# Performance work log

Hardware: AMD Instinct MI355X
Metric: run time of the kernel (lower is better)

## Reference

```python
import jax, jax.numpy as jnp
import numpy as np

B, S, E, H = 1, 4096, 768, 12
D = E // H  # head_dim = 64


def setup_inputs() -> dict:
    key = jax.random.key(0)
    ks = jax.random.split(key, 9)
    s = 1.0 / np.sqrt(E)
    return {
        "x": jax.random.normal(ks[0], (B, S, E), dtype=jnp.float32),
        "Wq": jax.random.uniform(ks[1], (E, E), jnp.float32, -s, s),
        "bq": jax.random.uniform(ks[2], (E,), jnp.float32, -s, s),
        "Wk": jax.random.uniform(ks[3], (E, E), jnp.float32, -s, s),
        "bk": jax.random.uniform(ks[4], (E,), jnp.float32, -s, s),
        "Wv": jax.random.uniform(ks[5], (E, E), jnp.float32, -s, s),
        "bv": jax.random.uniform(ks[6], (E,), jnp.float32, -s, s),
        "Wo": jax.random.uniform(ks[7], (E, E), jnp.float32, -s, s),
        "bo": jax.random.uniform(ks[8], (E,), jnp.float32, -s, s),
    }


def reference(x, Wq, bq, Wk, bk, Wv, bv, Wo, bo):
    b, s, e = x.shape
    # QKV projections, split heads -> [b, h, s, d]
    def split(t):
        return t.reshape(b, s, H, D).transpose(0, 2, 1, 3)
    q = split(x @ Wq.T + bq)
    k = split(x @ Wk.T + bk)
    v = split(x @ Wv.T + bv)
    scores = jnp.einsum("bhqd,bhkd->bhqk", q, k) / jnp.sqrt(jnp.float32(D))
    attn = jax.nn.softmax(scores, axis=-1)  # dropout is identity in eval
    out = jnp.einsum("bhqk,bhkd->bhqd", attn, v)
    out = out.transpose(0, 2, 1, 3).reshape(b, s, e)
    return out @ Wo.T + bo
```

## Files before the change

### kernel.cpp

```cpp
#include <hip/hip_runtime.h>
#include <hip/hip_bf16.h>
#include <math.h>

#define SEQ 4096
#define EDIM 768
#define NHEAD 12
#define HDIM 64
#define SE (SEQ * EDIM)
#define WMAT (EDIM * EDIM)
#define QSCALE 0.180336880111f

typedef __attribute__((ext_vector_type(8))) __bf16 bf16x8;
typedef __attribute__((ext_vector_type(4))) float f32x4;
typedef __attribute__((ext_vector_type(8))) unsigned short u16x8;
typedef unsigned short ushort_t;
typedef unsigned int uint_t;

#define MFMA16(a, b, c) __builtin_amdgcn_mfma_f32_16x16x32_bf16(a, b, c, 0, 0, 0)
#define GLOAD_LDS16(g, l)                                          \
  __builtin_amdgcn_global_load_lds(                                \
      (const __attribute__((address_space(1))) void*)(g),          \
      (__attribute__((address_space(3))) void*)(l), 16, 0, 0)

__device__ __forceinline__ unsigned short bfbits(float x) {
  return __builtin_bit_cast(unsigned short, (__bf16)x);
}
__device__ __forceinline__ void split1(float x, unsigned short* h,
                                       unsigned short* l) {
  __bf16 hb = (__bf16)x;
  *h = __builtin_bit_cast(unsigned short, hb);
  *l = __builtin_bit_cast(unsigned short, (__bf16)(x - (float)hb));
}
__device__ __forceinline__ bf16x8 ones8() {
  u16x8 u;
#pragma unroll
  for (int e = 0; e < 8; ++e) u[e] = 0x3F80;
  return __builtin_bit_cast(bf16x8, u);
}

__global__ __launch_bounds__(256) void wprep_kernel(
    const float* __restrict__ W0, const float* __restrict__ W1,
    const float* __restrict__ W2, const float* __restrict__ W3,
    ushort_t* __restrict__ WB, ushort_t* __restrict__ WOH,
    ushort_t* __restrict__ WOL) {
  const int m = blockIdx.y;
  const float* src = (m == 0) ? W0 : (m == 1) ? W1 : (m == 2) ? W2 : W3;
  const size_t i = ((size_t)blockIdx.x * 256 + threadIdx.x) * 8;
  float4 a = *(const float4*)(src + i);
  float4 b = *(const float4*)(src + i + 4);
  float fv[8] = {a.x, a.y, a.z, a.w, b.x, b.y, b.z, b.w};
  if (m < 3) {
    u16x8 hh;
#pragma unroll
    for (int e = 0; e < 8; ++e) hh[e] = bfbits(fv[e]);
    *(u16x8*)(WB + (size_t)m * WMAT + i) = hh;
  } else {
    u16x8 hh, ll;
#pragma unroll
    for (int e = 0; e < 8; ++e) {
      unsigned short x, y;
      split1(fv[e], &x, &y);
      hh[e] = x;
      ll[e] = y;
    }
    *(u16x8*)(WOH + i) = hh;
    *(u16x8*)(WOL + i) = ll;
  }
}

__global__ __launch_bounds__(256) void xprep_kernel(
    const float* __restrict__ x, ushort_t* __restrict__ xb) {
  const size_t i = ((size_t)blockIdx.x * 256 + threadIdx.x) * 8;
  float4 a = *(const float4*)(x + i);
  float4 b = *(const float4*)(x + i + 4);
  float fv[8] = {a.x, a.y, a.z, a.w, b.x, b.y, b.z, b.w};
  u16x8 hh;
#pragma unroll
  for (int e = 0; e < 8; ++e) hh[e] = bfbits(fv[e]);
  *(u16x8*)(xb + i) = hh;
}

__global__ __launch_bounds__(256) void qkv_kernel(
    const ushort_t* __restrict__ XB, const ushort_t* __restrict__ WB,
    const float* __restrict__ bq, const float* __restrict__ bk,
    const float* __restrict__ bv, ushort_t* __restrict__ QB,
    ushort_t* __restrict__ KB, ushort_t* __restrict__ VB) {
  __shared__ __align__(16) ushort_t AS[128][32];
  __shared__ __align__(16) ushort_t BS[128][32];

  const int z = blockIdx.z;
  const ushort_t* Bmat = WB + (size_t)z * WMAT;
  const float* bias = (z == 0) ? bq : (z == 1) ? bk : bv;
  ushort_t* outp = (z == 0) ? QB : (z == 1) ? KB : VB;
  const float scale = (z == 0) ? QSCALE : 1.0f;

  const int t = threadIdx.x;
  const int lane = t & 63;
  const int w = t >> 6;
  const int tn = t & 15;
  const int g = (t >> 4) & 3;
  const int wr = w >> 1, wc = w & 1;
  const int m0 = blockIdx.x * 128;
  const int n0 = blockIdx.y * 128;

  f32x4 acc[4][4];
#pragma unroll
  for (int mi = 0; mi < 4; ++mi)
#pragma unroll
    for (int nj = 0; nj < 4; ++nj) acc[mi][nj] = (f32x4){0.f, 0.f, 0.f, 0.f};

  const int crow = lane >> 2;
  const int ccol = (lane & 3) * 8;

  for (int k0 = 0; k0 < EDIM; k0 += 32) {
    __syncthreads();
#pragma unroll
    for (int i = 0; i < 2; ++i) {
      const int ch = w + 4 * i;
      const int row = ch * 16 + crow;
      GLOAD_LDS16(XB + (size_t)(m0 + row) * EDIM + k0 + ccol, &AS[ch * 16][0]);
      GLOAD_LDS16(Bmat + (size_t)(n0 + row) * EDIM + k0 + ccol, &BS[ch * 16][0]);
    }
    __syncthreads();

    bf16x8 ah[4], bh[4];
#pragma unroll
    for (int mi = 0; mi < 4; ++mi)
      ah[mi] = __builtin_bit_cast(
          bf16x8, *(const u16x8*)&AS[wr * 64 + mi * 16 + tn][8 * g]);
#pragma unroll
    for (int nj = 0; nj < 4; ++nj)
      bh[nj] = __builtin_bit_cast(
          bf16x8, *(const u16x8*)&BS[wc * 64 + nj * 16 + tn][8 * g]);
#pragma unroll
    for (int mi = 0; mi < 4; ++mi)
#pragma unroll
      for (int nj = 0; nj < 4; ++nj)
        acc[mi][nj] = MFMA16(ah[mi], bh[nj], acc[mi][nj]);
  }

#pragma unroll
  for (int mi = 0; mi < 4; ++mi) {
    const int rb = m0 + wr * 64 + mi * 16 + 4 * g;
#pragma unroll
    for (int nj = 0; nj < 4; ++nj) {
      const int col = n0 + wc * 64 + nj * 16 + tn;
      const float bb = bias[col];
#pragma unroll
      for (int r = 0; r < 4; ++r)
        outp[(size_t)(rb + r) * EDIM + col] =
            bfbits((acc[mi][nj][r] + bb) * scale);
    }
  }
}

__global__ __launch_bounds__(256) void proj_kernel(
    const ushort_t* __restrict__ Ah, const ushort_t* __restrict__ Al,
    const ushort_t* __restrict__ Bh, const ushort_t* __restrict__ Bl,
    const float* __restrict__ bias, float* __restrict__ outf) {
  __shared__ __align__(16) ushort_t AhS[128][32];
  __shared__ __align__(16) ushort_t AlS[128][32];
  __shared__ __align__(16) ushort_t BhS[128][32];
  __shared__ __align__(16) ushort_t BlS[128][32];

  const int t = threadIdx.x;
  const int lane = t & 63;
  const int w = t >> 6;
  const int tn = t & 15;
  const int g = (t >> 4) & 3;
  const int wr = w >> 1, wc = w & 1;
  const int m0 = blockIdx.x * 128;
  const int n0 = blockIdx.y * 128;

  f32x4 acc[4][4];
#pragma unroll
  for (int mi = 0; mi < 4; ++mi)
#pragma unroll
    for (int nj = 0; nj < 4; ++nj) acc[mi][nj] = (f32x4){0.f, 0.f, 0.f, 0.f};

  const int crow = lane >> 2;
  const int ccol = (lane & 3) * 8;

  for (int k0 = 0; k0 < EDIM; k0 += 32) {
    __syncthreads();
#pragma unroll
    for (int i = 0; i < 2; ++i) {
      const int ch = w + 4 * i;
      const int row = ch * 16 + crow;
      const size_t ga = (size_t)(m0 + row) * EDIM + k0 + ccol;
      const size_t gb = (size_t)(n0 + row) * EDIM + k0 + ccol;
      GLOAD_LDS16(Ah + ga, &AhS[ch * 16][0]);
      GLOAD_LDS16(Al + ga, &AlS[ch * 16][0]);
      GLOAD_LDS16(Bh + gb, &BhS[ch * 16][0]);
      GLOAD_LDS16(Bl + gb, &BlS[ch * 16][0]);
    }
    __syncthreads();

    bf16x8 ah[4], al[4], bh[4], bl[4];
#pragma unroll
    for (int mi = 0; mi < 4; ++mi) {
      ah[mi] = __builtin_bit_cast(
          bf16x8, *(const u16x8*)&AhS[wr * 64 + mi * 16 + tn][8 * g]);
      al[mi] = __builtin_bit_cast(
          bf16x8, *(const u16x8*)&AlS[wr * 64 + mi * 16 + tn][8 * g]);
    }
#pragma unroll
    for (int nj = 0; nj < 4; ++nj) {
      bh[nj] = __builtin_bit_cast(
          bf16x8, *(const u16x8*)&BhS[wc * 64 + nj * 16 + tn][8 * g]);
      bl[nj] = __builtin_bit_cast(
          bf16x8, *(const u16x8*)&BlS[wc * 64 + nj * 16 + tn][8 * g]);
    }
#pragma unroll
    for (int mi = 0; mi < 4; ++mi)
#pragma unroll
      for (int nj = 0; nj < 4; ++nj)
        acc[mi][nj] = MFMA16(ah[mi], bh[nj], acc[mi][nj]);
#pragma unroll
    for (int mi = 0; mi < 4; ++mi)
#pragma unroll
      for (int nj = 0; nj < 4; ++nj)
        acc[mi][nj] = MFMA16(al[mi], bh[nj], acc[mi][nj]);
#pragma unroll
    for (int mi = 0; mi < 4; ++mi)
#pragma unroll
      for (int nj = 0; nj < 4; ++nj)
        acc[mi][nj] = MFMA16(ah[mi], bl[nj], acc[mi][nj]);
  }

#pragma unroll
  for (int mi = 0; mi < 4; ++mi) {
    const int rb = m0 + wr * 64 + mi * 16 + 4 * g;
#pragma unroll
    for (int nj = 0; nj < 4; ++nj) {
      const int col = n0 + wc * 64 + nj * 16 + tn;
      const float bb = bias[col];
#pragma unroll
      for (int r = 0; r < 4; ++r)
        outf[(size_t)(rb + r) * EDIM + col] = acc[mi][nj][r] + bb;
    }
  }
}

__global__ __launch_bounds__(256) void attn_kernel(
    const ushort_t* __restrict__ QB, const ushort_t* __restrict__ KBg,
    const ushort_t* __restrict__ Vg, ushort_t* __restrict__ Ch_g,
    ushort_t* __restrict__ Cl_g) {
  constexpr int DP = HDIM + 8;
  __shared__ __align__(16) ushort_t KS[64][DP];
  __shared__ __align__(16) ushort_t Vt[HDIM][DP];
  __shared__ __align__(16) ushort_t Ps[4][16][DP];

  const int t = threadIdx.x;
  const int tn = t & 15;
  const int g = (t >> 4) & 3;
  const int kg = g * 8;
  const int wid = t >> 6;
  const int h = blockIdx.y;
  const int q0 = blockIdx.x * 64;
  const int hoff = h * HDIM;

  bf16x8 qb[2];
  {
    const size_t qoff = (size_t)(q0 + 16 * wid + tn) * EDIM + hoff;
#pragma unroll
    for (int st = 0; st < 2; ++st)
      qb[st] = __builtin_bit_cast(bf16x8,
                                  *(const u16x8*)(QB + qoff + 32 * st + kg));
  }

  const int kr = t >> 2;
  const int kc = (t & 3) * 16;
  const int vkey = (t & 31) * 2;
  const int vd0 = (t >> 5) * 8;

  u16x8 kh0, kh1, vv0, vv1;
  {
    const size_t ko = (size_t)kr * EDIM + hoff + kc;
    kh0 = *(const u16x8*)(KBg + ko);
    kh1 = *(const u16x8*)(KBg + ko + 8);
    const size_t vo = (size_t)vkey * EDIM + hoff + vd0;
    vv0 = *(const u16x8*)(Vg + vo);
    vv1 = *(const u16x8*)(Vg + vo + EDIM);
  }

  const bf16x8 ones = ones8();
  f32x4 o[4], lsum;
#pragma unroll
  for (int j = 0; j < 4; ++j) o[j] = (f32x4){0.f, 0.f, 0.f, 0.f};
  lsum = (f32x4){0.f, 0.f, 0.f, 0.f};

  for (int k0 = 0; k0 < SEQ; k0 += 64) {
    __syncthreads();
    *(u16x8*)&KS[kr][kc] = kh0;
    *(u16x8*)&KS[kr][kc + 8] = kh1;
#pragma unroll
    for (int i = 0; i < 8; ++i) {
      const uint_t wv = (uint_t)vv0[i] | ((uint_t)vv1[i] << 16);
      *(uint_t*)&Vt[vd0 + i][vkey] = wv;
    }
    if (k0 + 64 < SEQ) {
      const size_t ko = (size_t)(k0 + 64 + kr) * EDIM + hoff + kc;
      kh0 = *(const u16x8*)(KBg + ko);
      kh1 = *(const u16x8*)(KBg + ko + 8);
      const size_t vo = (size_t)(k0 + 64 + vkey) * EDIM + hoff + vd0;
      vv0 = *(const u16x8*)(Vg + vo);
      vv1 = *(const u16x8*)(Vg + vo + EDIM);
    }
    __syncthreads();

    f32x4 s[4];
#pragma unroll
    for (int j = 0; j < 4; ++j) s[j] = (f32x4){0.f, 0.f, 0.f, 0.f};
#pragma unroll
    for (int j = 0; j < 4; ++j)
#pragma unroll
      for (int st = 0; st < 2; ++st) {
        const bf16x8 kb = __builtin_bit_cast(
            bf16x8, *(const u16x8*)&KS[j * 16 + tn][32 * st + kg]);
        s[j] = MFMA16(qb[st], kb, s[j]);
      }

#pragma unroll
    for (int r = 0; r < 4; ++r)
#pragma unroll
      for (int j = 0; j < 4; ++j)
        Ps[wid][4 * g + r][16 * j + tn] = bfbits(exp2f(s[j][r]));

    bf16x8 pa[2];
#pragma unroll
    for (int st = 0; st < 2; ++st)
      pa[st] = __builtin_bit_cast(
          bf16x8, *(const u16x8*)&Ps[wid][tn][32 * st + kg]);
#pragma unroll
    for (int j = 0; j < 4; ++j)
#pragma unroll
      for (int st = 0; st < 2; ++st) {
        const bf16x8 vb = __builtin_bit_cast(
            bf16x8, *(const u16x8*)&Vt[j * 16 + tn][32 * st + kg]);
        o[j] = MFMA16(pa[st], vb, o[j]);
      }
    lsum = MFMA16(pa[0], ones, lsum);
    lsum = MFMA16(pa[1], ones, lsum);
  }

#pragma unroll
  for (int r = 0; r < 4; ++r) {
    const float inv = 1.f / lsum[r];
#pragma unroll
    for (int j = 0; j < 4; ++j) {
      const float val = o[j][r] * inv;
      unsigned short hh, ll;
      split1(val, &hh, &ll);
      const size_t idx =
          (size_t)(q0 + 16 * wid + 4 * g + r) * EDIM + hoff + 16 * j + tn;
      Ch_g[idx] = hh;
      Cl_g[idx] = ll;
    }
  }
}

extern "C" void kernel_launch(void* const* d_in, const int* in_sizes, int n_in,
                              void* d_out, int out_size, void* d_ws,
                              size_t ws_size, hipStream_t stream) {
  const float* x  = (const float*)d_in[0];
  const float* Wq = (const float*)d_in[1];
  const float* bq = (const float*)d_in[2];
  const float* Wk = (const float*)d_in[3];
  const float* bk = (const float*)d_in[4];
  const float* Wv = (const float*)d_in[5];
  const float* bv = (const float*)d_in[6];
  const float* Wo = (const float*)d_in[7];
  const float* bo = (const float*)d_in[8];
  float* out = (float*)d_out;

  ushort_t* WB  = (ushort_t*)d_ws;
  ushort_t* WOH = WB + (size_t)3 * WMAT;
  ushort_t* WOL = WOH + (size_t)WMAT;
  ushort_t* XB  = WOL + (size_t)WMAT;
  ushort_t* QB  = XB + (size_t)SE;
  ushort_t* KB  = QB + (size_t)SE;
  ushort_t* VB  = KB + (size_t)SE;
  ushort_t* CH  = VB + (size_t)SE;
  ushort_t* CL  = CH + (size_t)SE;

  dim3 gw(WMAT / 2048, 4);
  wprep_kernel<<<gw, 256, 0, stream>>>(Wq, Wk, Wv, Wo, WB, WOH, WOL);
  xprep_kernel<<<SE / 2048, 256, 0, stream>>>(x, XB);

  dim3 gq(SEQ / 128, EDIM / 128, 3);
  qkv_kernel<<<gq, 256, 0, stream>>>(XB, WB, bq, bk, bv, QB, KB, VB);

  dim3 ga(SEQ / 64, NHEAD);
  attn_kernel<<<ga, 256, 0, stream>>>(QB, KB, VB, CH, CL);

  dim3 go(SEQ / 128, EDIM / 128);
  proj_kernel<<<go, 256, 0, stream>>>(CH, CL, WOH, WOL, bo, out);
}
```

Measured before the change: 177.5 us.

## Halve attention block to two waves with 32 query rows each and double-buffered K/V

```diff
diff --git a/kernel.cpp b/kernel.cpp
--- a/kernel.cpp
+++ b/kernel.cpp
@@ -242,14 +242,14 @@
   }
 }
 
-__global__ __launch_bounds__(256) void attn_kernel(
+__global__ __launch_bounds__(128) void attn_kernel(
     const ushort_t* __restrict__ QB, const ushort_t* __restrict__ KBg,
     const ushort_t* __restrict__ Vg, ushort_t* __restrict__ Ch_g,
     ushort_t* __restrict__ Cl_g) {
   constexpr int DP = HDIM + 8;
-  __shared__ __align__(16) ushort_t KS[64][DP];
-  __shared__ __align__(16) ushort_t Vt[HDIM][DP];
-  __shared__ __align__(16) ushort_t Ps[4][16][DP];
+  __shared__ __align__(16) ushort_t KS[2][64][DP];
+  __shared__ __align__(16) ushort_t Vt[2][HDIM][DP];
+  __shared__ __align__(16) ushort_t Ps[2][32][DP];
 
   const int t = threadIdx.x;
   const int tn = t & 15;
@@ -260,104 +260,138 @@
   const int q0 = blockIdx.x * 64;
   const int hoff = h * HDIM;
 
-  bf16x8 qb[2];
+  bf16x8 qb[2][2];
+#pragma unroll
+  for (int rb = 0; rb < 2; ++rb) {
+    const size_t qoff =
+        (size_t)(q0 + 32 * wid + 16 * rb + tn) * EDIM + hoff;
+#pragma unroll
+    for (int st = 0; st < 2; ++st)
+      qb[rb][st] = __builtin_bit_cast(
+          bf16x8, *(const u16x8*)(QB + qoff + 32 * st + kg));
+  }
+
+  const int kr = t >> 1;
+  const int kc = (t & 1) * 32;
+  const int vkey = (t & 31) * 2;
+  const int vd0 = ((t >> 5) & 3) * 16;
+
+  u16x8 kreg[4], vreg[4];
   {
-    const size_t qoff = (size_t)(q0 + 16 * wid + tn) * EDIM + hoff;
-#pragma unroll
-    for (int st = 0; st < 2; ++st)
-      qb[st] = __builtin_bit_cast(bf16x8,
-                                  *(const u16x8*)(QB + qoff + 32 * st + kg));
-  }
-
-  const int kr = t >> 2;
-  const int kc = (t & 3) * 16;
-  const int vkey = (t & 31) * 2;
-  const int vd0 = (t >> 5) * 8;
-
-  u16x8 kh0, kh1, vv0, vv1;
-  {
-    const size_t ko = (size_t)kr * EDIM + hoff + kc;
-    kh0 = *(const u16x8*)(KBg + ko);
-    kh1 = *(const u16x8*)(KBg + ko + 8);
-    const size_t vo = (size_t)vkey * EDIM + hoff + vd0;
-    vv0 = *(const u16x8*)(Vg + vo);
-    vv1 = *(const u16x8*)(Vg + vo + EDIM);
+    const ushort_t* kp = KBg + (size_t)kr * EDIM + hoff + kc;
+    kreg[0] = *(const u16x8*)kp;
+    kreg[1] = *(const u16x8*)(kp + 8);
+    kreg[2] = *(const u16x8*)(kp + 16);
+    kreg[3] = *(const u16x8*)(kp + 24);
+    const ushort_t* vp = Vg + (size_t)vkey * EDIM + hoff + vd0;
+    vreg[0] = *(const u16x8*)vp;
+    vreg[1] = *(const u16x8*)(vp + 8);
+    vreg[2] = *(const u16x8*)(vp + EDIM);
+    vreg[3] = *(const u16x8*)(vp + EDIM + 8);
   }
 
   const bf16x8 ones = ones8();
-  f32x4 o[4], lsum;
-#pragma unroll
-  for (int j = 0; j < 4; ++j) o[j] = (f32x4){0.f, 0.f, 0.f, 0.f};
-  lsum = (f32x4){0.f, 0.f, 0.f, 0.f};
+  f32x4 o[2][4], lsum[2];
+#pragma unroll
+  for (int rb = 0; rb < 2; ++rb) {
+    lsum[rb] = (f32x4){0.f, 0.f, 0.f, 0.f};
+#pragma unroll
+    for (int j = 0; j < 4; ++j) o[rb][j] = (f32x4){0.f, 0.f, 0.f, 0.f};
+  }
 
   for (int k0 = 0; k0 < SEQ; k0 += 64) {
+    const int buf = (k0 >> 6) & 1;
+    *(u16x8*)&KS[buf][kr][kc] = kreg[0];
+    *(u16x8*)&KS[buf][kr][kc + 8] = kreg[1];
+    *(u16x8*)&KS[buf][kr][kc + 16] = kreg[2];
+    *(u16x8*)&KS[buf][kr][kc + 24] = kreg[3];
+#pragma unroll
+    for (int i = 0; i < 8; ++i) {
+      *(uint_t*)&Vt[buf][vd0 + i][vkey] =
+          (uint_t)vreg[0][i] | ((uint_t)vreg[2][i] << 16);
+      *(uint_t*)&Vt[buf][vd0 + 8 + i][vkey] =
+          (uint_t)vreg[1][i] | ((uint_t)vreg[3][i] << 16);
+    }
     __syncthreads();
-    *(u16x8*)&KS[kr][kc] = kh0;
-    *(u16x8*)&KS[kr][kc + 8] = kh1;
-#pragma unroll
-    for (int i = 0; i < 8; ++i) {
-      const uint_t wv = (uint_t)vv0[i] | ((uint_t)vv1[i] << 16);
-      *(uint_t*)&Vt[vd0 + i][vkey] = wv;
-    }
+
     if (k0 + 64 < SEQ) {
-      const size_t ko = (size_t)(k0 + 64 + kr) * EDIM + hoff + kc;
-      kh0 = *(const u16x8*)(KBg + ko);
-      kh1 = *(const u16x8*)(KBg + ko + 8);
-      const size_t vo = (size_t)(k0 + 64 + vkey) * EDIM + hoff + vd0;
-      vv0 = *(const u16x8*)(Vg + vo);
-      vv1 = *(const u16x8*)(Vg + vo + EDIM);
-    }
-    __syncthreads();
-
-    f32x4 s[4];
-#pragma unroll
-    for (int j = 0; j < 4; ++j) s[j] = (f32x4){0.f, 0.f, 0.f, 0.f};
+      const ushort_t* kp = KBg + (size_t)(k0 + 64 + kr) * EDIM + hoff + kc;
+      kreg[0] = *(const u16x8*)kp;
+      kreg[1] = *(const u16x8*)(kp + 8);
+      kreg[2] = *(const u16x8*)(kp + 16);
+      kreg[3] = *(const u16x8*)(kp + 24);
+      const ushort_t* vp =
+          Vg + (size_t)(k0 + 64 + vkey) * EDIM + hoff + vd0;
+      vreg[0] = *(const u16x8*)vp;
+      vreg[1] = *(const u16x8*)(vp + 8);
+      vreg[2] = *(const u16x8*)(vp + EDIM);
+      vreg[3] = *(const u16x8*)(vp + EDIM + 8);
+    }
+
+    f32x4 s[2][4];
+#pragma unroll
+    for (int rb = 0; rb < 2; ++rb)
+#pragma unroll
+      for (int j = 0; j < 4; ++j) s[rb][j] = (f32x4){0.f, 0.f, 0.f, 0.f};
 #pragma unroll
     for (int j = 0; j < 4; ++j)
 #pragma unroll
       for (int st = 0; st < 2; ++st) {
         const bf16x8 kb = __builtin_bit_cast(
-            bf16x8, *(const u16x8*)&KS[j * 16 + tn][32 * st + kg]);
-        s[j] = MFMA16(qb[st], kb, s[j]);
+            bf16x8, *(const u16x8*)&KS[buf][j * 16 + tn][32 * st + kg]);
+        s[0][j] = MFMA16(qb[0][st], kb, s[0][j]);
+        s[1][j] = MFMA16(qb[1][st], kb, s[1][j]);
       }
 
 #pragma unroll
-    for (int r = 0; r < 4; ++r)
-#pragma unroll
-      for (int j = 0; j < 4; ++j)
-        Ps[wid][4 * g + r][16 * j + tn] = bfbits(exp2f(s[j][r]));
-
-    bf16x8 pa[2];
-#pragma unroll
-    for (int st = 0; st < 2; ++st)
-      pa[st] = __builtin_bit_cast(
-          bf16x8, *(const u16x8*)&Ps[wid][tn][32 * st + kg]);
+    for (int rb = 0; rb < 2; ++rb)
+#pragma unroll
+      for (int r = 0; r < 4; ++r)
+#pragma unroll
+        for (int j = 0; j < 4; ++j)
+          Ps[wid][16 * rb + 4 * g + r][16 * j + tn] =
+              bfbits(exp2f(s[rb][j][r]));
+
+    bf16x8 pa[2][2];
+#pragma unroll
+    for (int rb = 0; rb < 2; ++rb)
+#pragma unroll
+      for (int st = 0; st < 2; ++st)
+        pa[rb][st] = __builtin_bit_cast(
+            bf16x8, *(const u16x8*)&Ps[wid][16 * rb + tn][32 * st + kg]);
 #pragma unroll
     for (int j = 0; j < 4; ++j)
 #pragma unroll
       for (int st = 0; st < 2; ++st) {
         const bf16x8 vb = __builtin_bit_cast(
-            bf16x8, *(const u16x8*)&Vt[j * 16 + tn][32 * st + kg]);
-        o[j] = MFMA16(pa[st], vb, o[j]);
+            bf16x8, *(const u16x8*)&Vt[buf][j * 16 + tn][32 * st + kg]);
+        o[0][j] = MFMA16(pa[0][st], vb, o[0][j]);
+        o[1][j] = MFMA16(pa[1][st], vb, o[1][j]);
       }
-    lsum = MFMA16(pa[0], ones, lsum);
-    lsum = MFMA16(pa[1], ones, lsum);
-  }
-
-#pragma unroll
-  for (int r = 0; r < 4; ++r) {
-    const float inv = 1.f / lsum[r];
-#pragma unroll
-    for (int j = 0; j < 4; ++j) {
-      const float val = o[j][r] * inv;
-      unsigned short hh, ll;
-      split1(val, &hh, &ll);
-      const size_t idx =
-          (size_t)(q0 + 16 * wid + 4 * g + r) * EDIM + hoff + 16 * j + tn;
-      Ch_g[idx] = hh;
-      Cl_g[idx] = ll;
-    }
-  }
+#pragma unroll
+    for (int rb = 0; rb < 2; ++rb) {
+      lsum[rb] = MFMA16(pa[rb][0], ones, lsum[rb]);
+      lsum[rb] = MFMA16(pa[rb][1], ones, lsum[rb]);
+    }
+  }
+
+#pragma unroll
+  for (int rb = 0; rb < 2; ++rb)
+#pragma unroll
+    for (int r = 0; r < 4; ++r) {
+      const float inv = 1.f / lsum[rb][r];
+#pragma unroll
+      for (int j = 0; j < 4; ++j) {
+        const float val = o[rb][j][r] * inv;
+        unsigned short hh, ll;
+        split1(val, &hh, &ll);
+        const size_t idx =
+            (size_t)(q0 + 32 * wid + 16 * rb + 4 * g + r) * EDIM + hoff +
+            16 * j + tn;
+        Ch_g[idx] = hh;
+        Cl_g[idx] = ll;
+      }
+    }
 }
 
 extern "C" void kernel_launch(void* const* d_in, const int* in_sizes, int n_in,
@@ -392,7 +426,7 @@
   qkv_kernel<<<gq, 256, 0, stream>>>(XB, WB, bq, bk, bv, QB, KB, VB);
 
   dim3 ga(SEQ / 64, NHEAD);
-  attn_kernel<<<ga, 256, 0, stream>>>(QB, KB, VB, CH, CL);
+  attn_kernel<<<ga, 128, 0, stream>>>(QB, KB, VB, CH, CL);
 
   dim3 go(SEQ / 128, EDIM / 128);
   proj_kernel<<<go, 256, 0, stream>>>(CH, CL, WOH, WOL, bo, out);
```

Result: slower. 204.6 us (+15.2%).

## Load K fragments directly from global into registers, compute transposed scores

Applied to the files above, without the earlier changes.

```diff
diff --git a/kernel.cpp b/kernel.cpp
--- a/kernel.cpp
+++ b/kernel.cpp
@@ -247,7 +247,6 @@
     const ushort_t* __restrict__ Vg, ushort_t* __restrict__ Ch_g,
     ushort_t* __restrict__ Cl_g) {
   constexpr int DP = HDIM + 8;
-  __shared__ __align__(16) ushort_t KS[64][DP];
   __shared__ __align__(16) ushort_t Vt[HDIM][DP];
   __shared__ __align__(16) ushort_t Ps[4][16][DP];
 
@@ -269,16 +268,11 @@
                                   *(const u16x8*)(QB + qoff + 32 * st + kg));
   }
 
-  const int kr = t >> 2;
-  const int kc = (t & 3) * 16;
   const int vkey = (t & 31) * 2;
   const int vd0 = (t >> 5) * 8;
 
-  u16x8 kh0, kh1, vv0, vv1;
+  u16x8 vv0, vv1;
   {
-    const size_t ko = (size_t)kr * EDIM + hoff + kc;
-    kh0 = *(const u16x8*)(KBg + ko);
-    kh1 = *(const u16x8*)(KBg + ko + 8);
     const size_t vo = (size_t)vkey * EDIM + hoff + vd0;
     vv0 = *(const u16x8*)(Vg + vo);
     vv1 = *(const u16x8*)(Vg + vo + EDIM);
@@ -291,18 +285,20 @@
   lsum = (f32x4){0.f, 0.f, 0.f, 0.f};
 
   for (int k0 = 0; k0 < SEQ; k0 += 64) {
-    __syncthreads();
-    *(u16x8*)&KS[kr][kc] = kh0;
-    *(u16x8*)&KS[kr][kc + 8] = kh1;
-#pragma unroll
-    for (int i = 0; i < 8; ++i) {
-      const uint_t wv = (uint_t)vv0[i] | ((uint_t)vv1[i] << 16);
-      *(uint_t*)&Vt[vd0 + i][vkey] = wv;
-    }
+    bf16x8 kc[4][2];
+#pragma unroll
+    for (int kb = 0; kb < 4; ++kb) {
+      const ushort_t* kp = KBg + (size_t)(k0 + 16 * kb + tn) * EDIM + hoff + kg;
+      kc[kb][0] = __builtin_bit_cast(bf16x8, *(const u16x8*)kp);
+      kc[kb][1] = __builtin_bit_cast(bf16x8, *(const u16x8*)(kp + 32));
+    }
+
+    __syncthreads();
+#pragma unroll
+    for (int i = 0; i < 8; ++i)
+      *(uint_t*)&Vt[vd0 + i][vkey] =
+          (uint_t)vv0[i] | ((uint_t)vv1[i] << 16);
     if (k0 + 64 < SEQ) {
-      const size_t ko = (size_t)(k0 + 64 + kr) * EDIM + hoff + kc;
-      kh0 = *(const u16x8*)(KBg + ko);
-      kh1 = *(const u16x8*)(KBg + ko + 8);
       const size_t vo = (size_t)(k0 + 64 + vkey) * EDIM + hoff + vd0;
       vv0 = *(const u16x8*)(Vg + vo);
       vv1 = *(const u16x8*)(Vg + vo + EDIM);
@@ -311,21 +307,23 @@
 
     f32x4 s[4];
 #pragma unroll
-    for (int j = 0; j < 4; ++j) s[j] = (f32x4){0.f, 0.f, 0.f, 0.f};
-#pragma unroll
-    for (int j = 0; j < 4; ++j)
-#pragma unroll
-      for (int st = 0; st < 2; ++st) {
-        const bf16x8 kb = __builtin_bit_cast(
-            bf16x8, *(const u16x8*)&KS[j * 16 + tn][32 * st + kg]);
-        s[j] = MFMA16(qb[st], kb, s[j]);
-      }
-
-#pragma unroll
-    for (int r = 0; r < 4; ++r)
-#pragma unroll
-      for (int j = 0; j < 4; ++j)
-        Ps[wid][4 * g + r][16 * j + tn] = bfbits(exp2f(s[j][r]));
+    for (int kb = 0; kb < 4; ++kb) {
+      s[kb] = (f32x4){0.f, 0.f, 0.f, 0.f};
+      s[kb] = MFMA16(kc[kb][0], qb[0], s[kb]);
+      s[kb] = MFMA16(kc[kb][1], qb[1], s[kb]);
+    }
+
+#pragma unroll
+    for (int kb = 0; kb < 4; ++kb) {
+      uint_t lo = (uint_t)bfbits(exp2f(s[kb][0])) |
+                  ((uint_t)bfbits(exp2f(s[kb][1])) << 16);
+      uint_t hi = (uint_t)bfbits(exp2f(s[kb][2])) |
+                  ((uint_t)bfbits(exp2f(s[kb][3])) << 16);
+      uint2 pk;
+      pk.x = lo;
+      pk.y = hi;
+      *(uint2*)&Ps[wid][tn][16 * kb + 4 * g] = pk;
+    }
 
     bf16x8 pa[2];
 #pragma unroll
```

After: 293.3 us. +65.2%, slower.
